# Kernel optimization log

Measured on AMD Instinct MI355X. Metric: run time of the kernel, lower is better.

## Reference

```python
import jax, jax.numpy as jnp
import numpy as np

B, N, D, E = 64, 1000, 128, 20000
NEG_SLOPE = 0.2   # GraphLayer leaky_relu negative_slope
BN_EPS = 1e-5


def setup_inputs() -> dict:
    key = jax.random.key(0)
    ks = jax.random.split(key, 16)
    data = jax.random.normal(ks[0], (B, N, D), jnp.float32)
    # edges with no self-loops (GraphLayer removes self-loops before re-adding them)
    dst = jax.random.randint(ks[1], (E,), 0, N)
    off = jax.random.randint(ks[2], (E,), 1, N)
    src = (dst + off) % N
    edge_index = jnp.stack([src, dst]).astype(jnp.int32)  # [2, E], row0=src(j), row1=dst(i)

    def p(k, shape, scale=0.05):
        return jax.random.normal(k, shape, jnp.float32) * scale

    return dict(
        data=data, edge_index=edge_index,
        emb=p(ks[3], (N, D), 0.1),
        lin_w=p(ks[4], (D, D)),
        att_i=p(ks[5], (D,)), att_j=p(ks[6], (D,)),
        att_em_i=p(ks[7], (D,)), att_em_j=p(ks[8], (D,)),
        gnn_bias=jnp.zeros((D,), jnp.float32),
        bn_gamma=jnp.ones((D,), jnp.float32),
        bn_beta=jnp.zeros((D,), jnp.float32),
        q_w=p(ks[9], (D, D)), q_b=jnp.zeros((D,), jnp.float32),
        k_w=p(ks[10], (D, D)), k_b=jnp.zeros((D,), jnp.float32),
        v_w=p(ks[11], (D, D)), v_b=jnp.zeros((D,), jnp.float32),
        temperature=jnp.asarray(np.sqrt(D), jnp.float32),
        f_w1=p(ks[12], (D, 2 * D)), f_b1=jnp.zeros((D,), jnp.float32),
        f_w2=p(ks[13], (D, D)), f_b2=jnp.zeros((D,), jnp.float32),
        out_w=p(ks[14], (1, D)), out_b=jnp.zeros((1,), jnp.float32),
    )


def _forward(data, emb, lin_w, att_i, att_j, att_em_i, att_em_j, gnn_bias,
             bn_gamma, bn_beta, q_w, q_b, k_w, k_b, v_w, v_b, temperature,
             f_w1, f_b1, f_w2, f_b2, out_w, out_b, edge_index):
    Bn = B * N
    # ---- temporal self-attention (seq_len == dim -> window of 1, per code constraint)
    xt = data.reshape(B, N, -1, D)                           # [B, N, W, D]
    q = xt @ q_w.T + q_b
    k = xt @ k_w.T + k_b
    v = xt @ v_w.T + v_b
    scores = jnp.einsum('bnwc,bnuc->bnwu', q, k) / (temperature + 1e-6)
    attn = jax.nn.softmax(scores, axis=-1)
    t_out = jnp.einsum('bnwu,bnuc->bnwc', attn, v).reshape(B, N, -1)

    # ---- spatial graph attention (GDN GraphLayer, heads=1, concat=False)
    x = data.reshape(Bn, -1) @ lin_w.T                       # [Bn, D]
    offs = jnp.arange(B, dtype=edge_index.dtype) * N         # get_batch_edge_index
    src = (edge_index[0][None, :] + offs[:, None]).reshape(-1)
    dst = (edge_index[1][None, :] + offs[:, None]).reshape(-1)
    loop = jnp.arange(Bn, dtype=edge_index.dtype)            # add_self_loops
    src = jnp.concatenate([src, loop])
    dst = jnp.concatenate([dst, loop])
    emb_full = jnp.tile(emb, (B, 1))                         # embedding tiled per graph
    # alpha_e = <[x_i|emb_i],[att_i|att_em_i]> + <[x_j|emb_j],[att_j|att_em_j]>
    node_i_score = x @ att_i + emb_full @ att_em_i           # [Bn]
    node_j_score = x @ att_j + emb_full @ att_em_j
    alpha = node_i_score[dst] + node_j_score[src]            # [E_total]
    alpha = jnp.where(alpha >= 0, alpha, NEG_SLOPE * alpha)  # leaky_relu(0.2)
    amax = jax.ops.segment_max(alpha, dst, num_segments=Bn)  # segment softmax over targets
    ex = jnp.exp(alpha - amax[dst])
    denom = jax.ops.segment_sum(ex, dst, num_segments=Bn)
    w = ex / denom[dst]
    agg = jax.ops.segment_sum(x[src] * w[:, None], dst, num_segments=Bn) + gnn_bias
    # BatchNorm1d (training-mode batch statistics, biased var) + ReLU
    mu = agg.mean(axis=0)
    var = agg.var(axis=0)
    s_out = jax.nn.relu(bn_gamma * (agg - mu) * jax.lax.rsqrt(var + BN_EPS) + bn_beta)
    s_out = s_out.reshape(B, N, -1)

    # ---- fusion MLP + OutLayer (layer_num=1 -> single Linear(D, 1))
    combined = jnp.concatenate([s_out, t_out], axis=-1)      # [B, N, 2D]
    fused = jax.nn.relu(combined @ f_w1.T + f_b1) @ f_w2.T + f_b2
    out = fused @ out_w.T + out_b                            # [B, N, 1]
    return out.reshape(Bn)


def reference(data, edge_index, emb, lin_w, att_i, att_j, att_em_i, att_em_j,
              gnn_bias, bn_gamma, bn_beta, q_w, q_b, k_w, k_b, v_w, v_b,
              temperature, f_w1, f_b1, f_w2, f_b2, out_w, out_b):
    return _forward(data, emb, lin_w, att_i, att_j, att_em_i, att_em_j, gnn_bias,
                    bn_gamma, bn_beta, q_w, q_b, k_w, k_b, v_w, v_b, temperature,
                    f_w1, f_b1, f_w2, f_b2, out_w, out_b, edge_index)
```

## Files before the change

### kernel.cpp

```cpp
#include <hip/hip_runtime.h>
#include <math.h>

constexpr int B_ = 64;
constexpr int N_ = 1000;
constexpr int D_ = 128;
constexpr int E_ = 20000;
constexpr int BN_TOT = B_ * N_;
constexpr float BN_EPS = 1e-5f;
constexpr float NEG_SLOPE = 0.2f;

typedef __attribute__((ext_vector_type(8))) __bf16 bf16x8;
typedef __attribute__((ext_vector_type(4))) float f32x4;
typedef __attribute__((ext_vector_type(2))) float f32x2;

__device__ __forceinline__ float leaky(float a) { return a >= 0.f ? a : NEG_SLOPE * a; }

__device__ __forceinline__ bf16x8 cvt8(const float* v) {
    bf16x8 h;
#pragma unroll
    for (int j = 0; j < 8; ++j) h[j] = (__bf16)v[j];
    return h;
}

__device__ __forceinline__ unsigned int packpair(float v, int l) {
    float vp = __shfl_xor(v, 1);
    __bf16 b0 = (__bf16)v, b1 = (__bf16)vp;
    unsigned int u0 = *(const unsigned short*)&b0;
    unsigned int u1 = *(const unsigned short*)&b1;
    return u0 | (u1 << 16);
}

__global__ __launch_bounds__(256) void k_prep(const float* __restrict__ lin_w,
                                              const float* __restrict__ v_w,
                                              const float* __restrict__ f_w1,
                                              const float* __restrict__ emb,
                                              const float* __restrict__ att_em_i,
                                              const float* __restrict__ att_em_j,
                                              const float* __restrict__ f_w2,
                                              const float* __restrict__ f_b2,
                                              const float* __restrict__ out_w,
                                              const float* __restrict__ out_b,
                                              __bf16* __restrict__ wcat_h, __bf16* __restrict__ wcat_l,
                                              __bf16* __restrict__ f1_h, __bf16* __restrict__ f1_l,
                                              float* __restrict__ eemi, float* __restrict__ eemj,
                                              float* __restrict__ g, float* __restrict__ c0,
                                              int* __restrict__ zbase) {
    const int blk = blockIdx.x;
    const int tid = threadIdx.x;
    if (blk < 256) {
        int i = blk * 256 + tid;
        if (i < 32768) {
            float v = (i < 16384) ? lin_w[i] : v_w[i - 16384];
            __bf16 h = (__bf16)v;
            wcat_h[i] = h;
            wcat_l[i] = (__bf16)(v - (float)h);
        } else {
            int j = i - 32768;
            float v = f_w1[j];
            __bf16 h = (__bf16)v;
            f1_h[j] = h;
            f1_l[j] = (__bf16)(v - (float)h);
        }
    } else if (blk == 256) {
        for (int k = tid; k < 2304; k += 256) zbase[k] = 0;
    } else if (blk == 257) {
        if (tid < 128) {
            float s = 0.f;
            for (int k = 0; k < D_; ++k) s += out_w[k] * f_w2[k * D_ + tid];
            g[tid] = s;
            if (tid == 0) {
                float c = out_b[0];
                for (int k = 0; k < D_; ++k) c += out_w[k] * f_b2[k];
                *c0 = c;
            }
        }
    } else {
        const int wid = tid >> 6;
        const int lane = tid & 63;
        const int n = (blk - 258) * 4 + wid;
        const float* er = emb + (size_t)n * D_;
        float e0 = er[lane], e1 = er[lane + 64];
        float si = e0 * att_em_i[lane] + e1 * att_em_i[lane + 64];
        float sj = e0 * att_em_j[lane] + e1 * att_em_j[lane + 64];
        for (int off = 32; off > 0; off >>= 1) {
            si += __shfl_down(si, off);
            sj += __shfl_down(sj, off);
        }
        if (lane == 0) { eemi[n] = si; eemj[n] = sj; }
    }
}

__global__ void k_count(const int* __restrict__ ei, int* __restrict__ offs) {
    int e = blockIdx.x * blockDim.x + threadIdx.x;
    if (e < E_) atomicAdd(&offs[ei[E_ + e] + 1], 1);
}

__global__ __launch_bounds__(1024) void k_scan(int* __restrict__ offs) {
    __shared__ int s[N_ + 1];
    int tid = threadIdx.x;
    if (tid <= N_) s[tid] = offs[tid];
    __syncthreads();
    for (int off = 1; off <= N_; off <<= 1) {
        int v = 0;
        if (tid <= N_) { v = s[tid]; if (tid >= off) v += s[tid - off]; }
        __syncthreads();
        if (tid <= N_) s[tid] = v;
        __syncthreads();
    }
    if (tid <= N_) offs[tid] = s[tid];
}

__global__ void k_scatter(const int* __restrict__ ei, const int* __restrict__ offs,
                          int* __restrict__ cursor, int* __restrict__ csr_src) {
    int e = blockIdx.x * blockDim.x + threadIdx.x;
    if (e < E_) {
        int dn = ei[E_ + e];
        int pos = offs[dn] + atomicAdd(&cursor[dn], 1);
        csr_src[pos] = ei[e];
    }
}

__global__ __launch_bounds__(512) void k_mfma_dual(const float* __restrict__ data,
                                                   const __bf16* __restrict__ wcat_h,
                                                   const __bf16* __restrict__ wcat_l,
                                                   const float* __restrict__ v_b,
                                                   const float* __restrict__ att_i,
                                                   const float* __restrict__ att_j,
                                                   const float* __restrict__ eemi,
                                                   const float* __restrict__ eemj,
                                                   float* __restrict__ ni,
                                                   float* __restrict__ nj,
                                                   unsigned int* __restrict__ xb,
                                                   unsigned int* __restrict__ tb) {
    const int tid = threadIdx.x;
    const int w = tid >> 6;
    const int l = tid & 63;
    bf16x8 Bh[2][4], Bl[2][4];
#pragma unroll
    for (int nt = 0; nt < 2; ++nt) {
        const int n = w * 32 + nt * 16 + (l & 15);
#pragma unroll
        for (int kk = 0; kk < 4; ++kk) {
            const int k = kk * 32 + (l >> 4) * 8;
            Bh[nt][kk] = *(const bf16x8*)&wcat_h[n * D_ + k];
            Bl[nt][kk] = *(const bf16x8*)&wcat_l[n * D_ + k];
        }
    }
    float vb[2] = {0.f, 0.f};
    float ai[2] = {0.f, 0.f}, aj[2] = {0.f, 0.f};
    if (w >= 4) {
#pragma unroll
        for (int nt = 0; nt < 2; ++nt) vb[nt] = v_b[w * 32 + nt * 16 + (l & 15) - 128];
    } else {
#pragma unroll
        for (int nt = 0; nt < 2; ++nt) {
            const int col = w * 32 + nt * 16 + (l & 15);
            ai[nt] = att_i[col];
            aj[nt] = att_j[col];
        }
    }
    __shared__ __align__(16) __bf16 dh[2][32 * D_];
    __shared__ float sred_i[4][32];
    __shared__ float sred_j[4][32];
    const int srow = tid >> 4;
    const int skq = (tid & 15) * 8;
    const int soff = srow * D_ + (skq ^ ((srow & 7) * 8));
    const int nchunks = BN_TOT / 32;
    float4 q0, q1;
    {
        const float* src = data + (size_t)(blockIdx.x * 32 + srow) * D_ + skq;
        q0 = *(const float4*)src;
        q1 = *(const float4*)(src + 4);
        float v[8] = {q0.x, q0.y, q0.z, q0.w, q1.x, q1.y, q1.z, q1.w};
        *(bf16x8*)&dh[0][soff] = cvt8(v);
    }
    int cur = 0;
    for (int ch = blockIdx.x; ch < nchunks; ch += gridDim.x) {
        const int nxt = ch + gridDim.x;
        if (nxt < nchunks) {
            const float* src = data + (size_t)(nxt * 32 + srow) * D_ + skq;
            q0 = *(const float4*)src;
            q1 = *(const float4*)(src + 4);
        }
        __syncthreads();
        f32x4 acc[2][2];
#pragma unroll
        for (int mt = 0; mt < 2; ++mt)
#pragma unroll
            for (int nt = 0; nt < 2; ++nt) acc[mt][nt] = (f32x4){0.f, 0.f, 0.f, 0.f};
#pragma unroll
        for (int mt = 0; mt < 2; ++mt) {
#pragma unroll
            for (int kk = 0; kk < 4; ++kk) {
                const int aidx = (mt * 16 + (l & 15)) * D_ + ((kk * 32 + (l >> 4) * 8) ^ ((l & 7) * 8));
                bf16x8 ah = *(const bf16x8*)&dh[cur][aidx];
#pragma unroll
                for (int nt = 0; nt < 2; ++nt) {
                    acc[mt][nt] = __builtin_amdgcn_mfma_f32_16x16x32_bf16(ah, Bh[nt][kk], acc[mt][nt], 0, 0, 0);
                    acc[mt][nt] = __builtin_amdgcn_mfma_f32_16x16x32_bf16(ah, Bl[nt][kk], acc[mt][nt], 0, 0, 0);
                }
            }
        }
        const int row0 = ch * 32;
        if (w < 4) {
            float pi[8], pj[8];
#pragma unroll
            for (int k2 = 0; k2 < 8; ++k2) { pi[k2] = 0.f; pj[k2] = 0.f; }
#pragma unroll
            for (int mt = 0; mt < 2; ++mt) {
#pragma unroll
                for (int nt = 0; nt < 2; ++nt) {
                    const int col = w * 32 + nt * 16 + (l & 15);
#pragma unroll
                    for (int r = 0; r < 4; ++r) {
                        float v = acc[mt][nt][r];
                        pi[mt * 4 + r] += v * ai[nt];
                        pj[mt * 4 + r] += v * aj[nt];
                        unsigned int u = packpair(v, l);
                        if (!(l & 1)) {
                            const int row = row0 + mt * 16 + (l >> 4) * 4 + r;
                            xb[(size_t)row * 64 + (col >> 1)] = u;
                        }
                    }
                }
            }
#pragma unroll
            for (int off = 1; off < 16; off <<= 1) {
#pragma unroll
                for (int k2 = 0; k2 < 8; ++k2) {
                    pi[k2] += __shfl_xor(pi[k2], off);
                    pj[k2] += __shfl_xor(pj[k2], off);
                }
            }
            if ((l & 15) == 0) {
#pragma unroll
                for (int mt = 0; mt < 2; ++mt)
#pragma unroll
                    for (int r = 0; r < 4; ++r) {
                        sred_i[w][mt * 16 + (l >> 4) * 4 + r] = pi[mt * 4 + r];
                        sred_j[w][mt * 16 + (l >> 4) * 4 + r] = pj[mt * 4 + r];
                    }
            }
        } else {
#pragma unroll
            for (int mt = 0; mt < 2; ++mt) {
#pragma unroll
                for (int nt = 0; nt < 2; ++nt) {
                    const int c2 = w * 32 + nt * 16 + (l & 15) - 128;
#pragma unroll
                    for (int r = 0; r < 4; ++r) {
                        float v = acc[mt][nt][r] + vb[nt];
                        unsigned int u = packpair(v, l);
                        if (!(l & 1)) {
                            const int row = row0 + mt * 16 + (l >> 4) * 4 + r;
                            tb[(size_t)row * 64 + (c2 >> 1)] = u;
                        }
                    }
                }
            }
        }
        __syncthreads();
        if (tid < 32) {
            const int row = row0 + tid;
            float si = sred_i[0][tid] + sred_i[1][tid] + sred_i[2][tid] + sred_i[3][tid];
            float sj = sred_j[0][tid] + sred_j[1][tid] + sred_j[2][tid] + sred_j[3][tid];
            const int n = row % N_;
            ni[row] = si + eemi[n];
            nj[row] = sj + eemj[n];
        }
        if (nxt < nchunks) {
            float v[8] = {q0.x, q0.y, q0.z, q0.w, q1.x, q1.y, q1.z, q1.w};
            *(bf16x8*)&dh[cur ^ 1][soff] = cvt8(v);
        }
        cur ^= 1;
    }
}

__global__ __launch_bounds__(256) void k_sagg(const unsigned int* __restrict__ xb,
                                              const int* __restrict__ offs,
                                              const int* __restrict__ csr_src,
                                              const float* __restrict__ ni,
                                              const float* __restrict__ nj,
                                              const float* __restrict__ gnn_bias,
                                              float* __restrict__ agg) {
    constexpr int CAP = 128;
    __shared__ int s_lds[4][CAP];
    __shared__ float w_lds[4][CAP];
    const int swz = (blockIdx.x & 7) * 2000 + (blockIdx.x >> 3);
    const int w = threadIdx.x >> 6;
    const int l = threadIdx.x & 63;
    const int bid = swz * 4 + w;
    const int b = bid / N_;
    const int i = bid - b * N_;
    const int base = b * N_;
    const int e0 = offs[i];
    const int deg = offs[i + 1] - e0;
    const int stg = deg < CAP ? deg : CAP;
    const float nii = ni[bid];
    const float aself = leaky(nii + nj[bid]);
    float aa0 = -1e30f, aa1 = -1e30f;
    if (l < stg) {
        int s = csr_src[e0 + l];
        s_lds[w][l] = s;
        aa0 = leaky(nii + nj[base + s]);
    }
    if (l + 64 < stg) {
        int s = csr_src[e0 + l + 64];
        s_lds[w][l + 64] = s;
        aa1 = leaky(nii + nj[base + s]);
    }
    float amax = fmaxf(aself, fmaxf(aa0, aa1));
    for (int e = e0 + CAP + l; e < e0 + deg; e += 64)
        amax = fmaxf(amax, leaky(nii + nj[base + csr_src[e]]));
    for (int off = 32; off > 0; off >>= 1) amax = fmaxf(amax, __shfl_xor(amax, off));
    const float se = __expf(aself - amax);
    float sum = 0.f;
    if (l < stg) { float ex = __expf(aa0 - amax); w_lds[w][l] = ex; sum += ex; }
    if (l + 64 < stg) { float ex = __expf(aa1 - amax); w_lds[w][l + 64] = ex; sum += ex; }
    for (int off = 32; off > 0; off >>= 1) sum += __shfl_xor(sum, off);
    float denom = se + sum;
    __syncthreads();
    float accx, accy;
    {
        unsigned int u = xb[(size_t)bid * 64 + l];
        accx = se * __uint_as_float(u << 16);
        accy = se * __uint_as_float(u & 0xffff0000u);
    }
    int k = 0;
    for (; k + 8 <= stg; k += 8) {
        unsigned int u[8];
        float wg[8];
#pragma unroll
        for (int j = 0; j < 8; ++j) {
            int s = s_lds[w][k + j];
            wg[j] = w_lds[w][k + j];
            u[j] = xb[(size_t)(base + s) * 64 + l];
        }
#pragma unroll
        for (int j = 0; j < 8; ++j) {
            accx += wg[j] * __uint_as_float(u[j] << 16);
            accy += wg[j] * __uint_as_float(u[j] & 0xffff0000u);
        }
    }
    for (; k < stg; ++k) {
        int s = s_lds[w][k];
        float wg = w_lds[w][k];
        unsigned int u = xb[(size_t)(base + s) * 64 + l];
        accx += wg * __uint_as_float(u << 16);
        accy += wg * __uint_as_float(u & 0xffff0000u);
    }
    for (int e = e0 + CAP; e < e0 + deg; ++e) {
        int s = csr_src[e];
        float wg = __expf(leaky(nii + nj[base + s]) - amax);
        unsigned int u = xb[(size_t)(base + s) * 64 + l];
        accx += wg * __uint_as_float(u << 16);
        accy += wg * __uint_as_float(u & 0xffff0000u);
        denom += wg;
    }
    const float dn = 1.f / denom;
    f32x2 gb = ((const f32x2*)gnn_bias)[l];
    f32x2 o;
    o.x = accx * dn + gb.x;
    o.y = accy * dn + gb.y;
    __builtin_nontemporal_store(o, (f32x2*)agg + (size_t)bid * 64 + l);
}

__global__ __launch_bounds__(256) void k_bn_part(const float* __restrict__ agg,
                                                 float* __restrict__ partials) {
    const int g = threadIdx.x >> 5;
    const int c4 = threadIdx.x & 31;
    f32x4 s = (f32x4){0.f, 0.f, 0.f, 0.f};
    f32x4 q = (f32x4){0.f, 0.f, 0.f, 0.f};
    for (int r = blockIdx.x * 8 + g; r < BN_TOT; r += 8192) {
        float4 v = *(const float4*)&agg[(size_t)r * D_ + c4 * 4];
        s.x += v.x; s.y += v.y; s.z += v.z; s.w += v.w;
        q.x += v.x * v.x; q.y += v.y * v.y; q.z += v.z * v.z; q.w += v.w * v.w;
    }
    __shared__ f32x4 ls[8][32];
    __shared__ f32x4 lq[8][32];
    ls[g][c4] = s;
    lq[g][c4] = q;
    __syncthreads();
    if (threadIdx.x < 32) {
        f32x4 ts = ls[0][threadIdx.x];
        f32x4 tq = lq[0][threadIdx.x];
#pragma unroll
        for (int gg = 1; gg < 8; ++gg) {
            f32x4 a = ls[gg][threadIdx.x];
            f32x4 b = lq[gg][threadIdx.x];
            ts.x += a.x; ts.y += a.y; ts.z += a.z; ts.w += a.w;
            tq.x += b.x; tq.y += b.y; tq.z += b.z; tq.w += b.w;
        }
        f32x4* p = (f32x4*)partials + (size_t)blockIdx.x * 64;
        p[threadIdx.x] = ts;
        p[32 + threadIdx.x] = tq;
    }
}

__global__ __launch_bounds__(1024) void k_bn_fin2(const float* __restrict__ partials,
                                                  const float* __restrict__ gamma,
                                                  const float* __restrict__ beta,
                                                  float* __restrict__ scale,
                                                  float* __restrict__ shift) {
    const int d = threadIdx.x & 127;
    const int part = threadIdx.x >> 7;
    float s = 0.f, q = 0.f;
    for (int blk = part * 128; blk < part * 128 + 128; ++blk) {
        s += partials[(size_t)blk * 256 + d];
        q += partials[(size_t)blk * 256 + 128 + d];
    }
    __shared__ float lss[8][128];
    __shared__ float lqq[8][128];
    lss[part][d] = s;
    lqq[part][d] = q;
    __syncthreads();
    if (threadIdx.x < 128) {
        float ts = 0.f, tq = 0.f;
#pragma unroll
        for (int p = 0; p < 8; ++p) { ts += lss[p][d]; tq += lqq[p][d]; }
        float mu = ts * (1.f / BN_TOT);
        float var = tq * (1.f / BN_TOT) - mu * mu;
        float sc = gamma[d] * rsqrtf(var + BN_EPS);
        scale[d] = sc;
        shift[d] = beta[d] - mu * sc;
    }
}

__global__ __launch_bounds__(512) void k_mfma_fusion(const float* __restrict__ agg,
                                                     const unsigned int* __restrict__ tb,
                                                     const __bf16* __restrict__ f1_h,
                                                     const __bf16* __restrict__ f1_l,
                                                     const float* __restrict__ f_b1,
                                                     const float* __restrict__ scale,
                                                     const float* __restrict__ shift,
                                                     const float* __restrict__ g,
                                                     const float* __restrict__ c0p,
                                                     float* __restrict__ out) {
    const int tid = threadIdx.x;
    const int w = tid >> 6;
    const int l = tid & 63;
    const float c0v = *c0p;
    bf16x8 Fh[8], Fl[8];
    const int ncol = w * 16 + (l & 15);
#pragma unroll
    for (int kk = 0; kk < 8; ++kk) {
        const int k = kk * 32 + (l >> 4) * 8;
        Fh[kk] = *(const bf16x8*)&f1_h[ncol * 256 + k];
        Fl[kk] = *(const bf16x8*)&f1_l[ncol * 256 + k];
    }
    const float b1c = f_b1[ncol];
    const float gc = g[ncol];
    __shared__ __align__(16) __bf16 ch_[2][32 * 256];
    __shared__ float part[8][32];
    const int srow = tid >> 4;
    const int scb = (tid & 15) * 16;
    const bool isagg = scb < 128;
    float4 sc4[4], sh4[4];
    if (isagg) {
#pragma unroll
        for (int q = 0; q < 4; ++q) {
            sc4[q] = *(const float4*)&scale[scb + q * 4];
            sh4[q] = *(const float4*)&shift[scb + q * 4];
        }
    }
    const int nchunks = BN_TOT / 32;
    float4 q[4];
    uint4 qu[2];
    auto loadc = [&](int chk) {
        if (isagg) {
            const float* srcp = agg + (size_t)(chk * 32 + srow) * D_ + scb;
#pragma unroll
            for (int qq = 0; qq < 4; ++qq) q[qq] = *(const float4*)(srcp + qq * 4);
        } else {
            const unsigned int* srcp = tb + (size_t)(chk * 32 + srow) * 64 + ((scb - 128) >> 1);
            qu[0] = *(const uint4*)srcp;
            qu[1] = *(const uint4*)(srcp + 4);
        }
    };
    auto storec = [&](int buf) {
        if (isagg) {
            float v[16];
#pragma unroll
            for (int qq = 0; qq < 4; ++qq) {
                float4 p = q[qq];
                p.x = fmaxf(p.x * sc4[qq].x + sh4[qq].x, 0.f);
                p.y = fmaxf(p.y * sc4[qq].y + sh4[qq].y, 0.f);
                p.z = fmaxf(p.z * sc4[qq].z + sh4[qq].z, 0.f);
                p.w = fmaxf(p.w * sc4[qq].w + sh4[qq].w, 0.f);
                v[qq * 4 + 0] = p.x; v[qq * 4 + 1] = p.y; v[qq * 4 + 2] = p.z; v[qq * 4 + 3] = p.w;
            }
#pragma unroll
            for (int hh = 0; hh < 2; ++hh) {
                const int c = scb + hh * 8;
                const int idx = srow * 256 + (c ^ ((srow & 7) * 8));
                *(bf16x8*)&ch_[buf][idx] = cvt8(v + hh * 8);
            }
        } else {
#pragma unroll
            for (int hh = 0; hh < 2; ++hh) {
                const int c = scb + hh * 8;
                const int idx = srow * 256 + (c ^ ((srow & 7) * 8));
                *(bf16x8*)&ch_[buf][idx] = *(const bf16x8*)&qu[hh];
            }
        }
    };
    loadc(blockIdx.x);
    storec(0);
    int cur = 0;
    for (int chk = blockIdx.x; chk < nchunks; chk += gridDim.x) {
        const int nxt = chk + gridDim.x;
        if (nxt < nchunks) loadc(nxt);
        __syncthreads();
#pragma unroll
        for (int mt = 0; mt < 2; ++mt) {
            f32x4 acc = (f32x4){0.f, 0.f, 0.f, 0.f};
#pragma unroll
            for (int kk = 0; kk < 8; ++kk) {
                const int ai = (mt * 16 + (l & 15)) * 256 + ((kk * 32 + (l >> 4) * 8) ^ ((l & 7) * 8));
                bf16x8 ah = *(const bf16x8*)&ch_[cur][ai];
                acc = __builtin_amdgcn_mfma_f32_16x16x32_bf16(ah, Fh[kk], acc, 0, 0, 0);
                acc = __builtin_amdgcn_mfma_f32_16x16x32_bf16(ah, Fl[kk], acc, 0, 0, 0);
            }
            float p[4];
#pragma unroll
            for (int r = 0; r < 4; ++r) p[r] = fmaxf(acc[r] + b1c, 0.f) * gc;
#pragma unroll
            for (int r = 0; r < 4; ++r) {
                p[r] += __shfl_xor(p[r], 1);
                p[r] += __shfl_xor(p[r], 2);
                p[r] += __shfl_xor(p[r], 4);
                p[r] += __shfl_xor(p[r], 8);
            }
            if ((l & 15) == 0) {
#pragma unroll
                for (int r = 0; r < 4; ++r) part[w][mt * 16 + (l >> 4) * 4 + r] = p[r];
            }
        }
        __syncthreads();
        if (tid < 32) {
            float s = c0v;
#pragma unroll
            for (int ww = 0; ww < 8; ++ww) s += part[ww][tid];
            out[chk * 32 + tid] = s;
        }
        if (nxt < nchunks) storec(cur ^ 1);
        cur ^= 1;
    }
}

extern "C" void kernel_launch(void* const* d_in, const int* in_sizes, int n_in,
                              void* d_out, int out_size, void* d_ws, size_t ws_size,
                              hipStream_t stream) {
    const float* data     = (const float*)d_in[0];
    const int*   ei       = (const int*)d_in[1];
    const float* emb      = (const float*)d_in[2];
    const float* lin_w    = (const float*)d_in[3];
    const float* att_i    = (const float*)d_in[4];
    const float* att_j    = (const float*)d_in[5];
    const float* att_em_i = (const float*)d_in[6];
    const float* att_em_j = (const float*)d_in[7];
    const float* gnn_bias = (const float*)d_in[8];
    const float* bn_gamma = (const float*)d_in[9];
    const float* bn_beta  = (const float*)d_in[10];
    const float* v_w      = (const float*)d_in[15];
    const float* v_b      = (const float*)d_in[16];
    const float* f_w1     = (const float*)d_in[18];
    const float* f_b1     = (const float*)d_in[19];
    const float* f_w2     = (const float*)d_in[20];
    const float* f_b2     = (const float*)d_in[21];
    const float* out_w    = (const float*)d_in[22];
    const float* out_b    = (const float*)d_in[23];
    float* out = (float*)d_out;

    float* ws = (float*)d_ws;
    float* x      = ws;
    float* tmat   = x + (size_t)BN_TOT * D_;
    float* agg    = tmat + (size_t)BN_TOT * D_;
    float* ni     = agg + (size_t)BN_TOT * D_;
    float* nj     = ni + BN_TOT;
    float* eemi   = nj + BN_TOT;
    float* eemj   = eemi + N_;
    float* g      = eemj + N_;
    float* c0     = g + D_;
    float* scale  = c0 + 8;
    float* shift  = scale + D_;
    int* offs     = (int*)(shift + D_);
    int* cursor   = offs + 1024;
    float* bn_sum = (float*)(cursor + 1024);
    float* bn_sq  = bn_sum + D_;
    int* csr_src  = (int*)(bn_sq + D_);
    float* exbuf  = (float*)(csr_src + E_);
    float* selfex = exbuf + (size_t)B_ * E_;
    float* denomv = selfex + BN_TOT;
    __bf16* wcat_h = (__bf16*)(denomv + BN_TOT);
    __bf16* wcat_l = wcat_h + 256 * 128;
    __bf16* f1_h   = wcat_l + 256 * 128;
    __bf16* f1_l   = f1_h + 128 * 256;
    float* partials = (float*)(f1_l + 128 * 256);
    unsigned int* xb = (unsigned int*)(partials + 1024 * 256);
    unsigned int* tb = (unsigned int*)tmat;

    k_prep<<<508, 256, 0, stream>>>(lin_w, v_w, f_w1, emb, att_em_i, att_em_j,
                                    f_w2, f_b2, out_w, out_b,
                                    wcat_h, wcat_l, f1_h, f1_l,
                                    eemi, eemj, g, c0, offs);
    k_count<<<(E_ + 255) / 256, 256, 0, stream>>>(ei, offs);
    k_scan<<<1, 1024, 0, stream>>>(offs);
    k_scatter<<<(E_ + 255) / 256, 256, 0, stream>>>(ei, offs, cursor, csr_src);
    k_mfma_dual<<<500, 512, 0, stream>>>(data, wcat_h, wcat_l, v_b,
                                         att_i, att_j, eemi, eemj,
                                         ni, nj, xb, tb);
    k_sagg<<<BN_TOT / 4, 256, 0, stream>>>(xb, offs, csr_src, ni, nj, gnn_bias, agg);
    k_bn_part<<<1024, 256, 0, stream>>>(agg, partials);
    k_bn_fin2<<<1, 1024, 0, stream>>>(partials, bn_gamma, bn_beta, scale, shift);
    k_mfma_fusion<<<500, 512, 0, stream>>>(agg, tb, f1_h, f1_l, f_b1, scale, shift, g, c0, out);
}
```

Before: 164.3 us.

## Fuse BatchNorm statistics into aggregation via sharded atomics, finalize in fusion kernel

```diff
diff --git a/kernel.cpp b/kernel.cpp
--- a/kernel.cpp
+++ b/kernel.cpp
@@ -62,7 +62,7 @@
             f1_l[j] = (__bf16)(v - (float)h);
         }
     } else if (blk == 256) {
-        for (int k = tid; k < 2304; k += 256) zbase[k] = 0;
+        for (int k = tid; k < 4096; k += 256) zbase[k] = 0;
     } else if (blk == 257) {
         if (tid < 128) {
             float s = 0.f;
@@ -282,10 +282,13 @@
                                               const float* __restrict__ ni,
                                               const float* __restrict__ nj,
                                               const float* __restrict__ gnn_bias,
-                                              float* __restrict__ agg) {
+                                              float* __restrict__ agg,
+                                              float* __restrict__ shadow) {
     constexpr int CAP = 128;
     __shared__ int s_lds[4][CAP];
     __shared__ float w_lds[4][CAP];
+    __shared__ f32x4 bns[4][32];
+    __shared__ f32x4 bnq[4][32];
     const int swz = (blockIdx.x & 7) * 2000 + (blockIdx.x >> 3);
     const int w = threadIdx.x >> 6;
     const int l = threadIdx.x & 63;
@@ -320,109 +323,102 @@
     for (int off = 32; off > 0; off >>= 1) sum += __shfl_xor(sum, off);
     float denom = se + sum;
     __syncthreads();
-    float accx, accy;
-    {
-        unsigned int u = xb[(size_t)bid * 64 + l];
-        accx = se * __uint_as_float(u << 16);
-        accy = se * __uint_as_float(u & 0xffff0000u);
+    const int hw = l >> 5;
+    const int c = l & 31;
+    const uint2* x2 = (const uint2*)xb;
+    f32x2 a01 = (f32x2){0.f, 0.f}, a23 = (f32x2){0.f, 0.f};
+    if (hw == 0) {
+        uint2 u = x2[(size_t)bid * 32 + c];
+        f32x2 v01, v23;
+        v01.x = __uint_as_float(u.x << 16); v01.y = __uint_as_float(u.x & 0xffff0000u);
+        v23.x = __uint_as_float(u.y << 16); v23.y = __uint_as_float(u.y & 0xffff0000u);
+        a01 += se * v01;
+        a23 += se * v23;
     }
     int k = 0;
     for (; k + 8 <= stg; k += 8) {
-        unsigned int u[8];
-        float wg[8];
-#pragma unroll
-        for (int j = 0; j < 8; ++j) {
-            int s = s_lds[w][k + j];
-            wg[j] = w_lds[w][k + j];
-            u[j] = xb[(size_t)(base + s) * 64 + l];
-        }
-#pragma unroll
-        for (int j = 0; j < 8; ++j) {
-            accx += wg[j] * __uint_as_float(u[j] << 16);
-            accy += wg[j] * __uint_as_float(u[j] & 0xffff0000u);
-        }
-    }
-    for (; k < stg; ++k) {
+        uint2 u[4];
+        float wg[4];
+#pragma unroll
+        for (int j = 0; j < 4; ++j) {
+            int e = k + j * 2 + hw;
+            int s = s_lds[w][e];
+            wg[j] = w_lds[w][e];
+            u[j] = x2[(size_t)(base + s) * 32 + c];
+        }
+#pragma unroll
+        for (int j = 0; j < 4; ++j) {
+            f32x2 v01, v23;
+            v01.x = __uint_as_float(u[j].x << 16); v01.y = __uint_as_float(u[j].x & 0xffff0000u);
+            v23.x = __uint_as_float(u[j].y << 16); v23.y = __uint_as_float(u[j].y & 0xffff0000u);
+            a01 += wg[j] * v01;
+            a23 += wg[j] * v23;
+        }
+    }
+    for (; k + 2 <= stg; k += 2) {
+        int e = k + hw;
+        int s = s_lds[w][e];
+        float wg = w_lds[w][e];
+        uint2 u = x2[(size_t)(base + s) * 32 + c];
+        f32x2 v01, v23;
+        v01.x = __uint_as_float(u.x << 16); v01.y = __uint_as_float(u.x & 0xffff0000u);
+        v23.x = __uint_as_float(u.y << 16); v23.y = __uint_as_float(u.y & 0xffff0000u);
+        a01 += wg * v01;
+        a23 += wg * v23;
+    }
+    if (k < stg && hw == 0) {
         int s = s_lds[w][k];
         float wg = w_lds[w][k];
-        unsigned int u = xb[(size_t)(base + s) * 64 + l];
-        accx += wg * __uint_as_float(u << 16);
-        accy += wg * __uint_as_float(u & 0xffff0000u);
+        uint2 u = x2[(size_t)(base + s) * 32 + c];
+        f32x2 v01, v23;
+        v01.x = __uint_as_float(u.x << 16); v01.y = __uint_as_float(u.x & 0xffff0000u);
+        v23.x = __uint_as_float(u.y << 16); v23.y = __uint_as_float(u.y & 0xffff0000u);
+        a01 += wg * v01;
+        a23 += wg * v23;
     }
     for (int e = e0 + CAP; e < e0 + deg; ++e) {
         int s = csr_src[e];
         float wg = __expf(leaky(nii + nj[base + s]) - amax);
-        unsigned int u = xb[(size_t)(base + s) * 64 + l];
-        accx += wg * __uint_as_float(u << 16);
-        accy += wg * __uint_as_float(u & 0xffff0000u);
+        if (hw == 0) {
+            uint2 u = x2[(size_t)(base + s) * 32 + c];
+            f32x2 v01, v23;
+            v01.x = __uint_as_float(u.x << 16); v01.y = __uint_as_float(u.x & 0xffff0000u);
+            v23.x = __uint_as_float(u.y << 16); v23.y = __uint_as_float(u.y & 0xffff0000u);
+            a01 += wg * v01;
+            a23 += wg * v23;
+        }
         denom += wg;
     }
-    const float dn = 1.f / denom;
-    f32x2 gb = ((const f32x2*)gnn_bias)[l];
-    f32x2 o;
-    o.x = accx * dn + gb.x;
-    o.y = accy * dn + gb.y;
-    __builtin_nontemporal_store(o, (f32x2*)agg + (size_t)bid * 64 + l);
-}
-
-__global__ __launch_bounds__(256) void k_bn_part(const float* __restrict__ agg,
-                                                 float* __restrict__ partials) {
-    const int g = threadIdx.x >> 5;
-    const int c4 = threadIdx.x & 31;
-    f32x4 s = (f32x4){0.f, 0.f, 0.f, 0.f};
-    f32x4 q = (f32x4){0.f, 0.f, 0.f, 0.f};
-    for (int r = blockIdx.x * 8 + g; r < BN_TOT; r += 8192) {
-        float4 v = *(const float4*)&agg[(size_t)r * D_ + c4 * 4];
-        s.x += v.x; s.y += v.y; s.z += v.z; s.w += v.w;
-        q.x += v.x * v.x; q.y += v.y * v.y; q.z += v.z * v.z; q.w += v.w * v.w;
-    }
-    __shared__ f32x4 ls[8][32];
-    __shared__ f32x4 lq[8][32];
-    ls[g][c4] = s;
-    lq[g][c4] = q;
+    a01.x += __shfl_xor(a01.x, 32);
+    a01.y += __shfl_xor(a01.y, 32);
+    a23.x += __shfl_xor(a23.x, 32);
+    a23.y += __shfl_xor(a23.y, 32);
+    if (hw == 0) {
+        const float dn = 1.f / denom;
+        f32x4 gb = ((const f32x4*)gnn_bias)[c];
+        f32x4 o;
+        o.x = a01.x * dn + gb.x;
+        o.y = a01.y * dn + gb.y;
+        o.z = a23.x * dn + gb.z;
+        o.w = a23.y * dn + gb.w;
+        __builtin_nontemporal_store(o, (f32x4*)agg + (size_t)bid * 32 + c);
+        bns[w][c] = o;
+        bnq[w][c] = o * o;
+    }
     __syncthreads();
     if (threadIdx.x < 32) {
-        f32x4 ts = ls[0][threadIdx.x];
-        f32x4 tq = lq[0][threadIdx.x];
-#pragma unroll
-        for (int gg = 1; gg < 8; ++gg) {
-            f32x4 a = ls[gg][threadIdx.x];
-            f32x4 b = lq[gg][threadIdx.x];
-            ts.x += a.x; ts.y += a.y; ts.z += a.z; ts.w += a.w;
-            tq.x += b.x; tq.y += b.y; tq.z += b.z; tq.w += b.w;
-        }
-        f32x4* p = (f32x4*)partials + (size_t)blockIdx.x * 64;
-        p[threadIdx.x] = ts;
-        p[32 + threadIdx.x] = tq;
-    }
-}
-
-__global__ __launch_bounds__(1024) void k_bn_fin2(const float* __restrict__ partials,
-                                                  const float* __restrict__ gamma,
-                                                  const float* __restrict__ beta,
-                                                  float* __restrict__ scale,
-                                                  float* __restrict__ shift) {
-    const int d = threadIdx.x & 127;
-    const int part = threadIdx.x >> 7;
-    float s = 0.f, q = 0.f;
-    for (int blk = part * 128; blk < part * 128 + 128; ++blk) {
-        s += partials[(size_t)blk * 256 + d];
-        q += partials[(size_t)blk * 256 + 128 + d];
-    }
-    __shared__ float lss[8][128];
-    __shared__ float lqq[8][128];
-    lss[part][d] = s;
-    lqq[part][d] = q;
-    __syncthreads();
-    if (threadIdx.x < 128) {
-        float ts = 0.f, tq = 0.f;
-#pragma unroll
-        for (int p = 0; p < 8; ++p) { ts += lss[p][d]; tq += lqq[p][d]; }
-        float mu = ts * (1.f / BN_TOT);
-        float var = tq * (1.f / BN_TOT) - mu * mu;
-        float sc = gamma[d] * rsqrtf(var + BN_EPS);
-        scale[d] = sc;
-        shift[d] = beta[d] - mu * sc;
+        const int cc = threadIdx.x;
+        f32x4 s = bns[0][cc] + bns[1][cc] + bns[2][cc] + bns[3][cc];
+        f32x4 q = bnq[0][cc] + bnq[1][cc] + bnq[2][cc] + bnq[3][cc];
+        float* sh = shadow + (blockIdx.x & 7) * 256;
+        atomicAdd(&sh[cc * 4 + 0], s.x);
+        atomicAdd(&sh[cc * 4 + 1], s.y);
+        atomicAdd(&sh[cc * 4 + 2], s.z);
+        atomicAdd(&sh[cc * 4 + 3], s.w);
+        atomicAdd(&sh[128 + cc * 4 + 0], q.x);
+        atomicAdd(&sh[128 + cc * 4 + 1], q.y);
+        atomicAdd(&sh[128 + cc * 4 + 2], q.z);
+        atomicAdd(&sh[128 + cc * 4 + 3], q.w);
     }
 }
 
@@ -431,8 +427,9 @@
                                                      const __bf16* __restrict__ f1_h,
                                                      const __bf16* __restrict__ f1_l,
                                                      const float* __restrict__ f_b1,
-                                                     const float* __restrict__ scale,
-                                                     const float* __restrict__ shift,
+                                                     const float* __restrict__ shadow,
+                                                     const float* __restrict__ gamma,
+                                                     const float* __restrict__ beta,
                                                      const float* __restrict__ g,
                                                      const float* __restrict__ c0p,
                                                      float* __restrict__ out) {
@@ -440,6 +437,20 @@
     const int w = tid >> 6;
     const int l = tid & 63;
     const float c0v = *c0p;
+    __shared__ float s_scale[128], s_shift[128];
+    if (tid < 128) {
+        float s = 0.f, q = 0.f;
+#pragma unroll
+        for (int k = 0; k < 8; ++k) {
+            s += shadow[k * 256 + tid];
+            q += shadow[k * 256 + 128 + tid];
+        }
+        float mu = s * (1.f / BN_TOT);
+        float var = q * (1.f / BN_TOT) - mu * mu;
+        float sc = gamma[tid] * rsqrtf(var + BN_EPS);
+        s_scale[tid] = sc;
+        s_shift[tid] = beta[tid] - mu * sc;
+    }
     bf16x8 Fh[8], Fl[8];
     const int ncol = w * 16 + (l & 15);
 #pragma unroll
@@ -455,12 +466,13 @@
     const int srow = tid >> 4;
     const int scb = (tid & 15) * 16;
     const bool isagg = scb < 128;
+    __syncthreads();
     float4 sc4[4], sh4[4];
     if (isagg) {
 #pragma unroll
         for (int q = 0; q < 4; ++q) {
-            sc4[q] = *(const float4*)&scale[scb + q * 4];
-            sh4[q] = *(const float4*)&shift[scb + q * 4];
+            sc4[q] = *(const float4*)&s_scale[scb + q * 4];
+            sh4[q] = *(const float4*)&s_shift[scb + q * 4];
         }
     }
     const int nchunks = BN_TOT / 32;
@@ -586,18 +598,13 @@
     float* shift  = scale + D_;
     int* offs     = (int*)(shift + D_);
     int* cursor   = offs + 1024;
-    float* bn_sum = (float*)(cursor + 1024);
-    float* bn_sq  = bn_sum + D_;
-    int* csr_src  = (int*)(bn_sq + D_);
-    float* exbuf  = (float*)(csr_src + E_);
-    float* selfex = exbuf + (size_t)B_ * E_;
-    float* denomv = selfex + BN_TOT;
-    __bf16* wcat_h = (__bf16*)(denomv + BN_TOT);
+    float* shadow = (float*)(cursor + 1024);
+    int* csr_src  = (int*)(shadow + 2048);
+    __bf16* wcat_h = (__bf16*)(csr_src + E_);
     __bf16* wcat_l = wcat_h + 256 * 128;
     __bf16* f1_h   = wcat_l + 256 * 128;
     __bf16* f1_l   = f1_h + 128 * 256;
-    float* partials = (float*)(f1_l + 128 * 256);
-    unsigned int* xb = (unsigned int*)(partials + 1024 * 256);
+    unsigned int* xb = (unsigned int*)(f1_l + 128 * 256);
     unsigned int* tb = (unsigned int*)tmat;
 
     k_prep<<<508, 256, 0, stream>>>(lin_w, v_w, f_w1, emb, att_em_i, att_em_j,
@@ -610,8 +617,7 @@
     k_mfma_dual<<<500, 512, 0, stream>>>(data, wcat_h, wcat_l, v_b,
                                          att_i, att_j, eemi, eemj,
                                          ni, nj, xb, tb);
-    k_sagg<<<BN_TOT / 4, 256, 0, stream>>>(xb, offs, csr_src, ni, nj, gnn_bias, agg);
-    k_bn_part<<<1024, 256, 0, stream>>>(agg, partials);
-    k_bn_fin2<<<1, 1024, 0, stream>>>(partials, bn_gamma, bn_beta, scale, shift);
-    k_mfma_fusion<<<500, 512, 0, stream>>>(agg, tb, f1_h, f1_l, f_b1, scale, shift, g, c0, out);
-}
+    k_sagg<<<BN_TOT / 4, 256, 0, stream>>>(xb, offs, csr_src, ni, nj, gnn_bias, agg, shadow);
+    k_mfma_fusion<<<500, 512, 0, stream>>>(agg, tb, f1_h, f1_l, f_b1, shadow,
+                                           bn_gamma, bn_beta, g, c0, out);
+}
```

Result: slower. 351.0 us (+113.7%).
